# Kernel optimization log

Measured on AMD Instinct MI355X. Metric: run time of the kernel, lower is better.

Reference implementation:

```python
import jax, jax.numpy as jnp
import numpy as np

B, S, D, H = 16, 512, 1024, 16
DH = D // H  # 64


def setup_inputs() -> dict:
    key = jax.random.key(0)
    kx, kq, kk, kv = jax.random.split(key, 4)
    stdv = 1.0 / np.sqrt(DH)  # reset_param uses 1/sqrt(t.size(1)) = 1/sqrt(head_dim)
    x = jax.random.normal(kx, (B, S, D), dtype=jnp.float32)
    Wq = jax.random.uniform(kq, (H, D, DH), dtype=jnp.float32, minval=-stdv, maxval=stdv)
    Wk = jax.random.uniform(kk, (H, D, DH), dtype=jnp.float32, minval=-stdv, maxval=stdv)
    Wv = jax.random.uniform(kv, (H, D, DH), dtype=jnp.float32, minval=-stdv, maxval=stdv)
    return {"x": x, "Wq": Wq, "Wk": Wk, "Wv": Wv}


def reference(x, Wq, Wk, Wv):
    # x: [B, S, D]; Wq/Wk/Wv: [H, D, DH] (stacked per-head params)
    q = jnp.einsum('bsd,hde->bhse', x, Wq)  # [B,H,S,DH]
    k = jnp.einsum('bsd,hde->bhse', x, Wk)
    v = jnp.einsum('bsd,hde->bhse', x, Wv)
    # NOTE: original scales by sqrt(input_dim), not sqrt(head_dim)
    scale = 1.0 / jnp.sqrt(jnp.float32(D))
    scores = jnp.einsum('bhse,bhte->bhst', q, k) * scale  # [B,H,S,S]
    attn = jax.nn.softmax(scores, axis=-1)
    out = jnp.einsum('bhst,bhte->bhse', attn, v)  # [B,H,S,DH]
    # concat heads along feature dim (head order matches torch cat over loop)
    return out.transpose(0, 2, 1, 3).reshape(x.shape[0], x.shape[1], D)
```

## Files before the change

### kernel.cpp

```cpp
#include <hip/hip_runtime.h>
#include <math.h>

constexpr int B = 16, S = 512, D = 1024, H = 16, DH = 64;
constexpr int BH = B * H;

typedef short bf16x8 __attribute__((ext_vector_type(8)));
typedef float f32x4  __attribute__((ext_vector_type(4)));

__device__ __forceinline__ unsigned short f2bf(float f) {
    unsigned u = __float_as_uint(f);
    u += 0x7fff + ((u >> 16) & 1);
    return (unsigned short)(u >> 16);
}

__global__ __launch_bounds__(256) void convert_xw(
    const float* __restrict__ x,
    const float* __restrict__ Wq, const float* __restrict__ Wk,
    const float* __restrict__ Wv,
    unsigned short* __restrict__ xb, unsigned short* __restrict__ WbT)
{
    __shared__ float tile[64][65];
    const int t = threadIdx.x;
    if (blockIdx.x < 8192) {
        int i = blockIdx.x * 256 + t;
        float4 v = ((const float4*)x)[i];
        ushort4 o;
        o.x = f2bf(v.x); o.y = f2bf(v.y); o.z = f2bf(v.z); o.w = f2bf(v.w);
        ((ushort4*)xb)[i] = o;
        return;
    }
    const int idx = blockIdx.x - 8192;
    const int d0 = (idx & 15) * 64;
    const int h = (idx >> 4) & 15;
    const int m = idx >> 8;
    const float* W = ((m == 0) ? Wq : (m == 1) ? Wk : Wv) + (size_t)h * D * DH;
    {
        int e = t & 63, dr = t >> 6;
        #pragma unroll
        for (int i = 0; i < 16; ++i) {
            int d = dr * 16 + i;
            tile[d][e] = W[(size_t)(d0 + d) * DH + e];
        }
    }
    __syncthreads();
    {
        int d = t & 63, er = t >> 6;
        unsigned short* out = WbT + (size_t)(m * H + h) * DH * D;
        #pragma unroll
        for (int i = 0; i < 16; ++i) {
            int e = er * 16 + i;
            out[(size_t)e * D + d0 + d] = f2bf(tile[d][e]);
        }
    }
}

__global__ __launch_bounds__(256) void qkv_gemm(
    const unsigned short* __restrict__ xb,
    const unsigned short* __restrict__ WbT,
    unsigned short* __restrict__ qkvb)
{
    __shared__ unsigned short As[128 * 64];
    __shared__ unsigned short Bs[128 * 64];

    const int t = threadIdx.x;
    const int w = t >> 6;
    const int wr = w >> 1, wc = w & 1;
    const int L = t & 63;
    const int lane15 = L & 15;
    const int quad = L >> 4;
    const int lrow8 = L >> 3;
    const int lg = L & 7;

    const int r0 = blockIdx.x * 128;
    const int n0 = blockIdx.y * 128;
    const int m  = n0 >> 10;

    f32x4 acc[4][4] = {};

    if (m == 2) {
        for (int k0 = 0; k0 < D; k0 += 64) {
            #pragma unroll
            for (int i = 0; i < 4; ++i) {
                int c = w * 4 + i;
                int r = c * 8 + lrow8;
                int gg = lg ^ (r & 7);
                const unsigned short* gp = xb + (size_t)(r0 + r) * D + k0 + gg * 8;
                __builtin_amdgcn_global_load_lds(
                    (const __attribute__((address_space(1))) void*)gp,
                    (__attribute__((address_space(3))) void*)(As + c * 512),
                    16, 0, 0);
                const unsigned short* gq = WbT + (size_t)(n0 + r) * D + k0 + gg * 8;
                __builtin_amdgcn_global_load_lds(
                    (const __attribute__((address_space(1))) void*)gq,
                    (__attribute__((address_space(3))) void*)(Bs + c * 512),
                    16, 0, 0);
            }
            __syncthreads();

            #pragma unroll
            for (int ks = 0; ks < 2; ++ks) {
                int gk = ks * 4 + quad;
                bf16x8 a[4], bb[4];
                #pragma unroll
                for (int rt = 0; rt < 4; ++rt) {
                    int ml = wr * 64 + rt * 16 + lane15;
                    a[rt] = *(const bf16x8*)(As + ml * 64 + ((gk ^ (ml & 7)) * 8));
                }
                #pragma unroll
                for (int ct = 0; ct < 4; ++ct) {
                    int nl = wc * 64 + ct * 16 + lane15;
                    bb[ct] = *(const bf16x8*)(Bs + nl * 64 + ((gk ^ (nl & 7)) * 8));
                }
                #pragma unroll
                for (int rt = 0; rt < 4; ++rt)
                    #pragma unroll
                    for (int ct = 0; ct < 4; ++ct)
                        acc[rt][ct] = __builtin_amdgcn_mfma_f32_16x16x32_bf16(
                            a[rt], bb[ct], acc[rt][ct], 0, 0, 0);
            }
            __syncthreads();
        }
    } else {
        for (int k0 = 0; k0 < D; k0 += 64) {
            #pragma unroll
            for (int i = 0; i < 4; ++i) {
                int c = w * 4 + i;
                int r = c * 8 + lrow8;
                int gg = lg ^ (r & 7);
                const unsigned short* gp = xb + (size_t)(r0 + r) * D + k0 + gg * 8;
                __builtin_amdgcn_global_load_lds(
                    (const __attribute__((address_space(1))) void*)gp,
                    (__attribute__((address_space(3))) void*)(As + c * 512),
                    16, 0, 0);
                const unsigned short* gq = WbT + (size_t)(n0 + r) * D + k0 + gg * 8;
                __builtin_amdgcn_global_load_lds(
                    (const __attribute__((address_space(1))) void*)gq,
                    (__attribute__((address_space(3))) void*)(Bs + c * 512),
                    16, 0, 0);
            }
            __syncthreads();

            #pragma unroll
            for (int ks = 0; ks < 2; ++ks) {
                int gk = ks * 4 + quad;
                bf16x8 a[4], bb[4];
                #pragma unroll
                for (int rt = 0; rt < 4; ++rt) {
                    int ml = wr * 64 + rt * 16 + lane15;
                    a[rt] = *(const bf16x8*)(As + ml * 64 + ((gk ^ (ml & 7)) * 8));
                }
                #pragma unroll
                for (int ct = 0; ct < 4; ++ct) {
                    int nl = wc * 64 + ct * 16 + lane15;
                    bb[ct] = *(const bf16x8*)(Bs + nl * 64 + ((gk ^ (nl & 7)) * 8));
                }
                #pragma unroll
                for (int rt = 0; rt < 4; ++rt)
                    #pragma unroll
                    for (int ct = 0; ct < 4; ++ct)
                        acc[rt][ct] = __builtin_amdgcn_mfma_f32_16x16x32_bf16(
                            bb[ct], a[rt], acc[rt][ct], 0, 0, 0);
            }
            __syncthreads();
        }
    }

    const int h  = ((n0 >> 6) + wc) & 15;
    const int bb_ = r0 >> 9;
    const int s0 = (r0 & 511) + wr * 64;

    if (m == 2) {
        unsigned short* outv = qkvb + ((size_t)(2 * BH) + (bb_ * H + h)) * (size_t)(S * DH);
        #pragma unroll
        for (int rt = 0; rt < 4; ++rt) {
            int srow = s0 + rt * 16 + quad * 4;
            #pragma unroll
            for (int ct = 0; ct < 4; ++ct) {
                int e = ct * 16 + lane15;
                ushort4 pk;
                pk.x = f2bf(acc[rt][ct][0]);
                pk.y = f2bf(acc[rt][ct][1]);
                pk.z = f2bf(acc[rt][ct][2]);
                pk.w = f2bf(acc[rt][ct][3]);
                *(ushort4*)(outv + (size_t)e * S + srow) = pk;
            }
        }
    } else {
        const float sc = (m == 0) ? 0.04508422002778011f : 1.0f;
        unsigned short* out = qkvb + ((size_t)m * BH + (bb_ * H + h)) * (size_t)(S * DH);
        #pragma unroll
        for (int rt = 0; rt < 4; ++rt) {
            int srow = s0 + rt * 16 + lane15;
            #pragma unroll
            for (int ct = 0; ct < 4; ++ct) {
                int e0 = ct * 16 + quad * 4;
                ushort4 pk;
                pk.x = f2bf(acc[rt][ct][0] * sc);
                pk.y = f2bf(acc[rt][ct][1] * sc);
                pk.z = f2bf(acc[rt][ct][2] * sc);
                pk.w = f2bf(acc[rt][ct][3] * sc);
                *(ushort4*)(out + (size_t)srow * DH + e0) = pk;
            }
        }
    }
}

__global__ __launch_bounds__(256) void attn_mfma(
    const unsigned short* __restrict__ qkvb, float* __restrict__ out)
{
    __shared__ unsigned short Qs[128 * 64];
    __shared__ unsigned short Ks[64 * 64];
    __shared__ unsigned short Vt[64 * 64];

    const int t = threadIdx.x;
    const int w = t >> 6;
    const int L = t & 63;
    const int lane15 = L & 15;
    const int quad = L >> 4;
    const int lrow8 = L >> 3;
    const int lg = L & 7;
    const int qr0 = blockIdx.x * 128;
    const int bh = blockIdx.y;
    const int b = bh >> 4, h = bh & 15;

    const unsigned short* qb = qkvb + (size_t)bh * S * DH;
    const unsigned short* kb = qkvb + (size_t)(BH + bh) * S * DH;
    const unsigned short* vt = qkvb + (size_t)(2 * BH + bh) * S * DH;

    #pragma unroll
    for (int i = 0; i < 4; ++i) {
        int base = w * 32 + i * 8;
        int r = base + lrow8;
        int gg = lg ^ (r & 7);
        const unsigned short* gp = qb + (size_t)(qr0 + r) * DH + gg * 8;
        __builtin_amdgcn_global_load_lds(
            (const __attribute__((address_space(1))) void*)gp,
            (__attribute__((address_space(3))) void*)(Qs + base * 64),
            16, 0, 0);
    }

    f32x4 o[2][4] = {};
    float plsum[2] = {0.f, 0.f};
    bf16x8 qf[2][2];

    for (int kt = 0; kt < S; kt += 64) {
        #pragma unroll
        for (int i = 0; i < 2; ++i) {
            int base = (w * 2 + i) * 8;
            int r = base + lrow8;
            int gr = (r & 32) | ((r & 12) << 1) | ((r & 16) >> 2) | (r & 3);
            int gg = lg ^ (r & 7);
            const unsigned short* gpk = kb + (size_t)(kt + gr) * DH + gg * 8;
            __builtin_amdgcn_global_load_lds(
                (const __attribute__((address_space(1))) void*)gpk,
                (__attribute__((address_space(3))) void*)(Ks + base * 64),
                16, 0, 0);
            const unsigned short* gpv = vt + (size_t)r * S + kt + gg * 8;
            __builtin_amdgcn_global_load_lds(
                (const __attribute__((address_space(1))) void*)gpv,
                (__attribute__((address_space(3))) void*)(Vt + base * 64),
                16, 0, 0);
        }
        __syncthreads();

        if (kt == 0) {
            #pragma unroll
            for (int mt = 0; mt < 2; ++mt)
                #pragma unroll
                for (int ks = 0; ks < 2; ++ks) {
                    int ml = w * 32 + mt * 16 + lane15;
                    int gk = ks * 4 + quad;
                    qf[mt][ks] = *(const bf16x8*)(Qs + ml * 64 + ((gk ^ (lane15 & 7)) * 8));
                }
        }

        f32x4 st[2][4] = {};
        #pragma unroll
        for (int ks = 0; ks < 2; ++ks) {
            int gk = ks * 4 + quad;
            bf16x8 kf[4];
            #pragma unroll
            for (int ct = 0; ct < 4; ++ct) {
                int kr = ct * 16 + lane15;
                kf[ct] = *(const bf16x8*)(Ks + kr * 64 + ((gk ^ (lane15 & 7)) * 8));
            }
            #pragma unroll
            for (int mt = 0; mt < 2; ++mt)
                #pragma unroll
                for (int ct = 0; ct < 4; ++ct)
                    st[mt][ct] = __builtin_amdgcn_mfma_f32_16x16x32_bf16(
                        kf[ct], qf[mt][ks], st[mt][ct], 0, 0, 0);
        }

        bf16x8 pB[2][2];
        #pragma unroll
        for (int mt = 0; mt < 2; ++mt) {
            float rs = 0.f;
            #pragma unroll
            for (int ct = 0; ct < 4; ++ct) {
                float p0 = exp2f(st[mt][ct][0]);
                float p1 = exp2f(st[mt][ct][1]);
                float p2 = exp2f(st[mt][ct][2]);
                float p3 = exp2f(st[mt][ct][3]);
                rs += (p0 + p1) + (p2 + p3);
                int hi = (ct & 1) * 4;
                pB[mt][ct >> 1][hi + 0] = (short)f2bf(p0);
                pB[mt][ct >> 1][hi + 1] = (short)f2bf(p1);
                pB[mt][ct >> 1][hi + 2] = (short)f2bf(p2);
                pB[mt][ct >> 1][hi + 3] = (short)f2bf(p3);
            }
            plsum[mt] += rs;
        }

        #pragma unroll
        for (int ks = 0; ks < 2; ++ks) {
            int gk = ks * 4 + quad;
            bf16x8 vf[4];
            #pragma unroll
            for (int nt = 0; nt < 4; ++nt) {
                int dh = nt * 16 + lane15;
                vf[nt] = *(const bf16x8*)(Vt + dh * 64 + ((gk ^ (lane15 & 7)) * 8));
            }
            #pragma unroll
            for (int mt = 0; mt < 2; ++mt)
                #pragma unroll
                for (int nt = 0; nt < 4; ++nt)
                    o[mt][nt] = __builtin_amdgcn_mfma_f32_16x16x32_bf16(
                        vf[nt], pB[mt][ks], o[mt][nt], 0, 0, 0);
        }
        __syncthreads();
    }

    #pragma unroll
    for (int mt = 0; mt < 2; ++mt) {
        float l = plsum[mt];
        l += __shfl_xor(l, 16, 64);
        l += __shfl_xor(l, 32, 64);
        float inv = 1.0f / l;
        int srow = qr0 + w * 32 + mt * 16 + lane15;
        float* op = out + (size_t)(b * S + srow) * D + h * DH;
        #pragma unroll
        for (int nt = 0; nt < 4; ++nt) {
            float4 v;
            v.x = o[mt][nt][0] * inv;
            v.y = o[mt][nt][1] * inv;
            v.z = o[mt][nt][2] * inv;
            v.w = o[mt][nt][3] * inv;
            *(float4*)(op + nt * 16 + quad * 4) = v;
        }
    }
}

extern "C" void kernel_launch(void* const* d_in, const int* in_sizes, int n_in,
                              void* d_out, int out_size, void* d_ws, size_t ws_size,
                              hipStream_t stream) {
    const float* x  = (const float*)d_in[0];
    const float* Wq = (const float*)d_in[1];
    const float* Wk = (const float*)d_in[2];
    const float* Wv = (const float*)d_in[3];
    float* outp = (float*)d_out;

    unsigned short* qkvb = (unsigned short*)d_ws;
    unsigned short* xb   = (unsigned short*)((char*)d_ws + 50331648);
    unsigned short* WbT  = (unsigned short*)((char*)d_ws + 67108864);

    convert_xw<<<dim3(8192 + 768), 256, 0, stream>>>(x, Wq, Wk, Wv, xb, WbT);
    qkv_gemm<<<dim3(B * S / 128, 3 * H * DH / 128), 256, 0, stream>>>(xb, WbT, qkvb);
    attn_mfma<<<dim3(S / 128, BH), 256, 0, stream>>>(qkvb, outp);
}
```

Before: 201.8 us.

## Load Q/K/V fragments directly from global into registers, dropping LDS staging

The attention kernel no longer stages Q, K and V tiles through shared memory with global_load_lds and barriers. Each wave now loads its MFMA operand fragments straight from global memory (relying on L1/L2 for reuse across the four waves), and the kernel adds a launch-bounds occupancy hint of 3 blocks. This removes the LDS traffic and both __syncthreads per key tile. In exchange it issues redundant global loads per wave, has no explicit prefetch overlap, and may raise register pressure.

Measured after the change: 227.9 us. 12.9% more time.

```diff
diff --git a/kernel.cpp b/kernel.cpp
--- a/kernel.cpp
+++ b/kernel.cpp
@@ -205,20 +205,14 @@
     }
 }
 
-__global__ __launch_bounds__(256) void attn_mfma(
+__global__ __launch_bounds__(256, 3) void attn_mfma(
     const unsigned short* __restrict__ qkvb, float* __restrict__ out)
 {
-    __shared__ unsigned short Qs[128 * 64];
-    __shared__ unsigned short Ks[64 * 64];
-    __shared__ unsigned short Vt[64 * 64];
-
     const int t = threadIdx.x;
     const int w = t >> 6;
     const int L = t & 63;
     const int lane15 = L & 15;
     const int quad = L >> 4;
-    const int lrow8 = L >> 3;
-    const int lg = L & 7;
     const int qr0 = blockIdx.x * 128;
     const int bh = blockIdx.y;
     const int b = bh >> 4, h = bh & 15;
@@ -227,70 +221,46 @@
     const unsigned short* kb = qkvb + (size_t)(BH + bh) * S * DH;
     const unsigned short* vt = qkvb + (size_t)(2 * BH + bh) * S * DH;
 
+    bf16x8 qf[2][2];
     #pragma unroll
-    for (int i = 0; i < 4; ++i) {
-        int base = w * 32 + i * 8;
-        int r = base + lrow8;
-        int gg = lg ^ (r & 7);
-        const unsigned short* gp = qb + (size_t)(qr0 + r) * DH + gg * 8;
-        __builtin_amdgcn_global_load_lds(
-            (const __attribute__((address_space(1))) void*)gp,
-            (__attribute__((address_space(3))) void*)(Qs + base * 64),
-            16, 0, 0);
-    }
+    for (int mt = 0; mt < 2; ++mt)
+        #pragma unroll
+        for (int ks = 0; ks < 2; ++ks) {
+            int row = qr0 + w * 32 + mt * 16 + lane15;
+            qf[mt][ks] = *(const bf16x8*)(qb + (size_t)row * DH + ks * 32 + quad * 8);
+        }
+
+    const int kbase = ((lane15 >> 2) << 3) | (lane15 & 3);
 
     f32x4 o[2][4] = {};
     float plsum[2] = {0.f, 0.f};
-    bf16x8 qf[2][2];
 
     for (int kt = 0; kt < S; kt += 64) {
-        #pragma unroll
-        for (int i = 0; i < 2; ++i) {
-            int base = (w * 2 + i) * 8;
-            int r = base + lrow8;
-            int gr = (r & 32) | ((r & 12) << 1) | ((r & 16) >> 2) | (r & 3);
-            int gg = lg ^ (r & 7);
-            const unsigned short* gpk = kb + (size_t)(kt + gr) * DH + gg * 8;
-            __builtin_amdgcn_global_load_lds(
-                (const __attribute__((address_space(1))) void*)gpk,
-                (__attribute__((address_space(3))) void*)(Ks + base * 64),
-                16, 0, 0);
-            const unsigned short* gpv = vt + (size_t)r * S + kt + gg * 8;
-            __builtin_amdgcn_global_load_lds(
-                (const __attribute__((address_space(1))) void*)gpv,
-                (__attribute__((address_space(3))) void*)(Vt + base * 64),
-                16, 0, 0);
-        }
-        __syncthreads();
-
-        if (kt == 0) {
-            #pragma unroll
-            for (int mt = 0; mt < 2; ++mt)
-                #pragma unroll
-                for (int ks = 0; ks < 2; ++ks) {
-                    int ml = w * 32 + mt * 16 + lane15;
-                    int gk = ks * 4 + quad;
-                    qf[mt][ks] = *(const bf16x8*)(Qs + ml * 64 + ((gk ^ (lane15 & 7)) * 8));
-                }
+        bf16x8 kf[2][4];
+        #pragma unroll
+        for (int ct = 0; ct < 4; ++ct) {
+            int key = kt + ((ct >> 1) << 5) + ((ct & 1) << 2) + kbase;
+            const unsigned short* kp = kb + (size_t)key * DH + quad * 8;
+            kf[0][ct] = *(const bf16x8*)(kp);
+            kf[1][ct] = *(const bf16x8*)(kp + 32);
+        }
+        bf16x8 vf[2][4];
+        #pragma unroll
+        for (int nt = 0; nt < 4; ++nt) {
+            const unsigned short* vp = vt + (size_t)(nt * 16 + lane15) * S + kt + quad * 8;
+            vf[0][nt] = *(const bf16x8*)(vp);
+            vf[1][nt] = *(const bf16x8*)(vp + 32);
         }
 
         f32x4 st[2][4] = {};
         #pragma unroll
-        for (int ks = 0; ks < 2; ++ks) {
-            int gk = ks * 4 + quad;
-            bf16x8 kf[4];
-            #pragma unroll
-            for (int ct = 0; ct < 4; ++ct) {
-                int kr = ct * 16 + lane15;
-                kf[ct] = *(const bf16x8*)(Ks + kr * 64 + ((gk ^ (lane15 & 7)) * 8));
-            }
+        for (int ks = 0; ks < 2; ++ks)
             #pragma unroll
             for (int mt = 0; mt < 2; ++mt)
                 #pragma unroll
                 for (int ct = 0; ct < 4; ++ct)
                     st[mt][ct] = __builtin_amdgcn_mfma_f32_16x16x32_bf16(
-                        kf[ct], qf[mt][ks], st[mt][ct], 0, 0, 0);
-        }
+                        kf[ks][ct], qf[mt][ks], st[mt][ct], 0, 0, 0);
 
         bf16x8 pB[2][2];
         #pragma unroll
@@ -313,22 +283,13 @@
         }
 
         #pragma unroll
-        for (int ks = 0; ks < 2; ++ks) {
-            int gk = ks * 4 + quad;
-            bf16x8 vf[4];
-            #pragma unroll
-            for (int nt = 0; nt < 4; ++nt) {
-                int dh = nt * 16 + lane15;
-                vf[nt] = *(const bf16x8*)(Vt + dh * 64 + ((gk ^ (lane15 & 7)) * 8));
-            }
+        for (int ksg = 0; ksg < 2; ++ksg)
             #pragma unroll
             for (int mt = 0; mt < 2; ++mt)
                 #pragma unroll
                 for (int nt = 0; nt < 4; ++nt)
                     o[mt][nt] = __builtin_amdgcn_mfma_f32_16x16x32_bf16(
-                        vf[nt], pB[mt][ks], o[mt][nt], 0, 0, 0);
-        }
-        __syncthreads();
+                        vf[ksg][nt], pB[mt][ksg], o[mt][nt], 0, 0, 0);
     }
 
     #pragma unroll
```

## Load Q fragments directly to registers and double the K/V tile to 128

Applied to the files above, without the earlier changes.

Q fragments are now read straight from global memory into registers instead of being staged through shared memory. The K and V shared-memory tiles grow from 64 to 128 keys, each with its own XOR swizzle, and each staged tile is processed as two 64-key halves. This halves the number of outer iterations and block-wide barriers per query tile. In exchange the kernel issues uncoalesced per-lane Q loads and uses the same total shared memory, now split between K and V instead of Q, K and V.

Result: no change. 204.5 us (+1.4%).

```diff
diff --git a/kernel.cpp b/kernel.cpp
--- a/kernel.cpp
+++ b/kernel.cpp
@@ -208,9 +208,8 @@
 __global__ __launch_bounds__(256) void attn_mfma(
     const unsigned short* __restrict__ qkvb, float* __restrict__ out)
 {
-    __shared__ unsigned short Qs[128 * 64];
-    __shared__ unsigned short Ks[64 * 64];
-    __shared__ unsigned short Vt[64 * 64];
+    __shared__ unsigned short Ks[128 * 64];
+    __shared__ unsigned short Vt[64 * 128];
 
     const int t = threadIdx.x;
     const int w = t >> 6;
@@ -227,106 +226,103 @@
     const unsigned short* kb = qkvb + (size_t)(BH + bh) * S * DH;
     const unsigned short* vt = qkvb + (size_t)(2 * BH + bh) * S * DH;
 
+    bf16x8 qf[2][2];
     #pragma unroll
-    for (int i = 0; i < 4; ++i) {
-        int base = w * 32 + i * 8;
-        int r = base + lrow8;
-        int gg = lg ^ (r & 7);
-        const unsigned short* gp = qb + (size_t)(qr0 + r) * DH + gg * 8;
-        __builtin_amdgcn_global_load_lds(
-            (const __attribute__((address_space(1))) void*)gp,
-            (__attribute__((address_space(3))) void*)(Qs + base * 64),
-            16, 0, 0);
-    }
+    for (int mt = 0; mt < 2; ++mt)
+        #pragma unroll
+        for (int ks = 0; ks < 2; ++ks) {
+            int row = qr0 + w * 32 + mt * 16 + lane15;
+            qf[mt][ks] = *(const bf16x8*)(qb + (size_t)row * DH + ks * 32 + quad * 8);
+        }
 
     f32x4 o[2][4] = {};
     float plsum[2] = {0.f, 0.f};
-    bf16x8 qf[2][2];
-
-    for (int kt = 0; kt < S; kt += 64) {
-        #pragma unroll
-        for (int i = 0; i < 2; ++i) {
-            int base = (w * 2 + i) * 8;
-            int r = base + lrow8;
-            int gr = (r & 32) | ((r & 12) << 1) | ((r & 16) >> 2) | (r & 3);
+
+    for (int kt = 0; kt < S; kt += 128) {
+        #pragma unroll
+        for (int i = 0; i < 4; ++i) {
+            int c = w * 4 + i;
+            int r = c * 8 + lrow8;
+            int r6 = r & 63;
+            int gr = (r & 64) | (r6 & 32) | ((r6 & 12) << 1) | ((r6 & 16) >> 2) | (r6 & 3);
             int gg = lg ^ (r & 7);
             const unsigned short* gpk = kb + (size_t)(kt + gr) * DH + gg * 8;
             __builtin_amdgcn_global_load_lds(
                 (const __attribute__((address_space(1))) void*)gpk,
-                (__attribute__((address_space(3))) void*)(Ks + base * 64),
+                (__attribute__((address_space(3))) void*)(Ks + r * 64 - lrow8 * 64 + lrow8 * 64),
                 16, 0, 0);
-            const unsigned short* gpv = vt + (size_t)r * S + kt + gg * 8;
+        }
+        #pragma unroll
+        for (int i = 0; i < 4; ++i) {
+            int c = w * 4 + i;
+            int dh = c * 4 + (L >> 4);
+            int p  = L & 15;
+            int d  = p ^ (dh & 15);
+            const unsigned short* gpv = vt + (size_t)dh * S + kt + d * 8;
             __builtin_amdgcn_global_load_lds(
                 (const __attribute__((address_space(1))) void*)gpv,
-                (__attribute__((address_space(3))) void*)(Vt + base * 64),
+                (__attribute__((address_space(3))) void*)(Vt + c * 512),
                 16, 0, 0);
         }
         __syncthreads();
 
-        if (kt == 0) {
-            #pragma unroll
-            for (int mt = 0; mt < 2; ++mt)
-                #pragma unroll
-                for (int ks = 0; ks < 2; ++ks) {
-                    int ml = w * 32 + mt * 16 + lane15;
-                    int gk = ks * 4 + quad;
-                    qf[mt][ks] = *(const bf16x8*)(Qs + ml * 64 + ((gk ^ (lane15 & 7)) * 8));
-                }
-        }
-
-        f32x4 st[2][4] = {};
-        #pragma unroll
-        for (int ks = 0; ks < 2; ++ks) {
-            int gk = ks * 4 + quad;
-            bf16x8 kf[4];
-            #pragma unroll
-            for (int ct = 0; ct < 4; ++ct) {
-                int kr = ct * 16 + lane15;
-                kf[ct] = *(const bf16x8*)(Ks + kr * 64 + ((gk ^ (lane15 & 7)) * 8));
-            }
-            #pragma unroll
-            for (int mt = 0; mt < 2; ++mt)
-                #pragma unroll
-                for (int ct = 0; ct < 4; ++ct)
-                    st[mt][ct] = __builtin_amdgcn_mfma_f32_16x16x32_bf16(
-                        kf[ct], qf[mt][ks], st[mt][ct], 0, 0, 0);
-        }
-
-        bf16x8 pB[2][2];
-        #pragma unroll
-        for (int mt = 0; mt < 2; ++mt) {
-            float rs = 0.f;
-            #pragma unroll
-            for (int ct = 0; ct < 4; ++ct) {
-                float p0 = exp2f(st[mt][ct][0]);
-                float p1 = exp2f(st[mt][ct][1]);
-                float p2 = exp2f(st[mt][ct][2]);
-                float p3 = exp2f(st[mt][ct][3]);
-                rs += (p0 + p1) + (p2 + p3);
-                int hi = (ct & 1) * 4;
-                pB[mt][ct >> 1][hi + 0] = (short)f2bf(p0);
-                pB[mt][ct >> 1][hi + 1] = (short)f2bf(p1);
-                pB[mt][ct >> 1][hi + 2] = (short)f2bf(p2);
-                pB[mt][ct >> 1][hi + 3] = (short)f2bf(p3);
-            }
-            plsum[mt] += rs;
-        }
-
-        #pragma unroll
-        for (int ks = 0; ks < 2; ++ks) {
-            int gk = ks * 4 + quad;
-            bf16x8 vf[4];
-            #pragma unroll
-            for (int nt = 0; nt < 4; ++nt) {
-                int dh = nt * 16 + lane15;
-                vf[nt] = *(const bf16x8*)(Vt + dh * 64 + ((gk ^ (lane15 & 7)) * 8));
-            }
-            #pragma unroll
-            for (int mt = 0; mt < 2; ++mt)
-                #pragma unroll
-                for (int nt = 0; nt < 4; ++nt)
-                    o[mt][nt] = __builtin_amdgcn_mfma_f32_16x16x32_bf16(
-                        vf[nt], pB[mt][ks], o[mt][nt], 0, 0, 0);
+        #pragma unroll
+        for (int hh = 0; hh < 2; ++hh) {
+            f32x4 st[2][4] = {};
+            #pragma unroll
+            for (int ks = 0; ks < 2; ++ks) {
+                int gk = ks * 4 + quad;
+                bf16x8 kf[4];
+                #pragma unroll
+                for (int ct = 0; ct < 4; ++ct) {
+                    int kr = hh * 64 + ct * 16 + lane15;
+                    kf[ct] = *(const bf16x8*)(Ks + kr * 64 + ((gk ^ (kr & 7)) * 8));
+                }
+                #pragma unroll
+                for (int mt = 0; mt < 2; ++mt)
+                    #pragma unroll
+                    for (int ct = 0; ct < 4; ++ct)
+                        st[mt][ct] = __builtin_amdgcn_mfma_f32_16x16x32_bf16(
+                            kf[ct], qf[mt][ks], st[mt][ct], 0, 0, 0);
+            }
+
+            bf16x8 pB[2][2];
+            #pragma unroll
+            for (int mt = 0; mt < 2; ++mt) {
+                float rs = 0.f;
+                #pragma unroll
+                for (int ct = 0; ct < 4; ++ct) {
+                    float p0 = exp2f(st[mt][ct][0]);
+                    float p1 = exp2f(st[mt][ct][1]);
+                    float p2 = exp2f(st[mt][ct][2]);
+                    float p3 = exp2f(st[mt][ct][3]);
+                    rs += (p0 + p1) + (p2 + p3);
+                    int hi = (ct & 1) * 4;
+                    pB[mt][ct >> 1][hi + 0] = (short)f2bf(p0);
+                    pB[mt][ct >> 1][hi + 1] = (short)f2bf(p1);
+                    pB[mt][ct >> 1][hi + 2] = (short)f2bf(p2);
+                    pB[mt][ct >> 1][hi + 3] = (short)f2bf(p3);
+                }
+                plsum[mt] += rs;
+            }
+
+            #pragma unroll
+            for (int ksg = 0; ksg < 2; ++ksg) {
+                bf16x8 vf[4];
+                #pragma unroll
+                for (int nt = 0; nt < 4; ++nt) {
+                    int dh = nt * 16 + lane15;
+                    int kg = hh * 8 + ksg * 4 + quad;
+                    int p  = kg ^ (dh & 15);
+                    vf[nt] = *(const bf16x8*)(Vt + dh * 128 + p * 8);
+                }
+                #pragma unroll
+                for (int mt = 0; mt < 2; ++mt)
+                    #pragma unroll
+                    for (int nt = 0; nt < 4; ++nt)
+                        o[mt][nt] = __builtin_amdgcn_mfma_f32_16x16x32_bf16(
+                            vf[nt], pB[mt][ksg], o[mt][nt], 0, 0, 0);
+            }
         }
         __syncthreads();
     }
```
